# Performance work log

Measured on AMD Instinct MI355X. Metric: run time of the kernel, lower is better.

## Reference

```python
import jax, jax.numpy as jnp
import numpy as np

NUM_HEADS = 12
D_MODEL = 768
D_HEAD = D_MODEL // NUM_HEADS


def setup_inputs() -> dict:
    key = jax.random.key(0)
    k_x, k_wqkv, k_bqkv, k_wo, k_bo = jax.random.split(key, 5)
    B, S = 1, 4096
    x = jax.random.normal(k_x, (B, S, D_MODEL), dtype=jnp.float32)
    # flax Dense default init: lecun_normal for kernel, zeros for bias
    w_qkv = jax.random.normal(k_wqkv, (D_MODEL, 3 * D_MODEL), dtype=jnp.float32) / np.sqrt(D_MODEL)
    b_qkv = jnp.zeros((3 * D_MODEL,), dtype=jnp.float32)
    w_o = jax.random.normal(k_wo, (D_MODEL, D_MODEL), dtype=jnp.float32) / np.sqrt(D_MODEL)
    b_o = jnp.zeros((D_MODEL,), dtype=jnp.float32)
    return {"x": x, "w_qkv": w_qkv, "b_qkv": b_qkv, "w_o": w_o, "b_o": b_o}


def reference(x, w_qkv, b_qkv, w_o, b_o):
    B, S, _ = x.shape
    H, Dh = NUM_HEADS, D_HEAD
    qkv = jnp.einsum('bsd,de->bse', x, w_qkv) + b_qkv  # [B,S,3*D]
    q, k, v = jnp.split(qkv, 3, axis=-1)
    # [B,S,D] -> [B,H,S,Dh]
    q = q.reshape(B, S, H, Dh).transpose(0, 2, 1, 3)
    k = k.reshape(B, S, H, Dh).transpose(0, 2, 1, 3)
    v = v.reshape(B, S, H, Dh).transpose(0, 2, 1, 3)
    logits = jnp.einsum('bhqd,bhkd->bhqk', q, k) / jnp.sqrt(jnp.float32(Dh))
    weights = jax.nn.softmax(logits, axis=-1)  # deterministic=True -> no dropout
    attn = jnp.einsum('bhqk,bhkd->bhqd', weights, v)
    attn = attn.transpose(0, 2, 1, 3).reshape(B, S, H * Dh)
    return jnp.einsum('bsd,de->bse', attn, w_o) + b_o
```

## Files before the change

kernel.cpp:

```cpp
#include <hip/hip_runtime.h>

typedef unsigned short u16;
typedef __attribute__((ext_vector_type(8))) short bf16x8;
typedef __attribute__((ext_vector_type(4))) float f32x4;

#define CST 0.18033688011112042f

__device__ inline u16 f2bf(float f) {
    unsigned u;
    __builtin_memcpy(&u, &f, 4);
    unsigned r = (u + 0x7FFF + ((u >> 16) & 1)) >> 16;
    return (u16)r;
}
__device__ inline unsigned pack2(float lo, float hi) {
    return (unsigned)f2bf(lo) | ((unsigned)f2bf(hi) << 16);
}
__device__ inline unsigned fbits(float f) {
    unsigned u;
    __builtin_memcpy(&u, &f, 4);
    return u;
}
__device__ inline f32x4 fzero() {
    f32x4 z = {0.f, 0.f, 0.f, 0.f};
    return z;
}
__device__ inline f32x4 mfma16(bf16x8 a, bf16x8 b, f32x4 c) {
    return __builtin_amdgcn_mfma_f32_16x16x32_bf16(a, b, c, 0, 0, 0);
}

__device__ inline void gld_lds16(const u16* g, u16* l) {
    __builtin_amdgcn_global_load_lds(
        reinterpret_cast<const __attribute__((address_space(1))) unsigned int*>(
            reinterpret_cast<uintptr_t>(g)),
        reinterpret_cast<__attribute__((address_space(3))) unsigned int*>(
            static_cast<unsigned int>(reinterpret_cast<uintptr_t>(l))),
        16, 0, 0);
}

#define NB_WQKV (72 * 24)
#define NB_WO   (24 * 24)
#define NB_CVT  (4096 * 768 / 2048)

__global__ __launch_bounds__(256) void prep(const float* __restrict__ x,
                                            const float* __restrict__ w_qkv,
                                            const float* __restrict__ w_o,
                                            u16* __restrict__ xb,
                                            u16* __restrict__ wqkvT,
                                            u16* __restrict__ woT) {
    __shared__ float tile[32][33];
    int bid = blockIdx.x;
    int t = threadIdx.x;
    if (bid < NB_WQKV + NB_WO) {
        const float* in;
        u16* out;
        int bx, by, R, C;
        if (bid < NB_WQKV) {
            in = w_qkv; out = wqkvT; R = 768; C = 2304;
            bx = bid % 72; by = bid / 72;
        } else {
            int b2 = bid - NB_WQKV;
            in = w_o; out = woT; R = 768; C = 768;
            bx = b2 % 24; by = b2 / 24;
        }
        int c0 = bx * 32, r0 = by * 32;
        int tx = t & 31, ty = t >> 5;
#pragma unroll
        for (int j = 0; j < 32; j += 8)
            tile[ty + j][tx] = in[(size_t)(r0 + ty + j) * C + c0 + tx];
        __syncthreads();
#pragma unroll
        for (int j = 0; j < 32; j += 8)
            out[(size_t)(c0 + ty + j) * R + r0 + tx] = f2bf(tile[tx][ty + j]);
    } else {
        int i = (bid - NB_WQKV - NB_WO) * 2048 + t * 8;
        float4 a = *(const float4*)(x + i);
        float4 b = *(const float4*)(x + i + 4);
        uint4 w;
        w.x = pack2(a.x, a.y);
        w.y = pack2(a.z, a.w);
        w.z = pack2(b.x, b.y);
        w.w = pack2(b.z, b.w);
        *(uint4*)(xb + i) = w;
    }
}

__global__ __launch_bounds__(256) void vtrans(const u16* __restrict__ qkv,
                                              u16* __restrict__ vt) {
    __shared__ u16 T[64 * 136];
    int t = threadIdx.x;
    int h = blockIdx.y, kv0 = blockIdx.x * 128;
    {
        int key = t >> 1, ch = (t & 1) * 32;
        const u16* vp = qkv + (size_t)(kv0 + key) * 2304 + 1536 + h * 64 + ch;
        u16 tmp[32];
        *(uint4*)&tmp[0]  = *(const uint4*)vp;
        *(uint4*)&tmp[8]  = *(const uint4*)(vp + 8);
        *(uint4*)&tmp[16] = *(const uint4*)(vp + 16);
        *(uint4*)&tmp[24] = *(const uint4*)(vp + 24);
        int k5 = key & 31, grp = key >> 5;
        int kp = (grp << 5) | (((k5 >> 2) & 3) << 3) | ((k5 >> 4) << 2) | (k5 & 3);
#pragma unroll
        for (int j = 0; j < 32; j++) T[(ch + j) * 136 + kp] = tmp[j];
    }
    __syncthreads();
    {
        int dh = t >> 2, kc = (t & 3) * 32;
        uint4 o0 = *(const uint4*)&T[dh * 136 + kc];
        uint4 o1 = *(const uint4*)&T[dh * 136 + kc + 8];
        uint4 o2 = *(const uint4*)&T[dh * 136 + kc + 16];
        uint4 o3 = *(const uint4*)&T[dh * 136 + kc + 24];
        u16* op = vt + ((size_t)(h * 64 + dh)) * 4096 + kv0 + kc;
        *(uint4*)op = o0;
        *(uint4*)(op + 8) = o1;
        *(uint4*)(op + 16) = o2;
        *(uint4*)(op + 24) = o3;
    }
}

template <int MT, bool OUT_F32, bool SCALE_Q>
__global__ __launch_bounds__(256) void gemm_bt(const u16* __restrict__ A,
                                               const u16* __restrict__ Bt,
                                               const float* __restrict__ bias,
                                               void* __restrict__ Cv,
                                               int M, int N, int K) {
    constexpr int MI = MT / 32;
    constexpr int NA = MT / 64;
    constexpr int AH = MT * 32;
    constexpr int BH = 128 * 32;
    __shared__ u16 As[2 * AH];
    __shared__ u16 Bs[2 * BH];

    int t = threadIdx.x;
    int wave = t >> 6, lane = t & 63, quad = lane >> 4, l16 = lane & 15;
    int mbase = blockIdx.y * MT, nbase = blockIdx.x * 128;
    int mw = (wave & 1) * (MT / 2), nw = (wave >> 1) * 64;

    f32x4 acc[MI][4];
#pragma unroll
    for (int i = 0; i < MI; i++)
#pragma unroll
        for (int j = 0; j < 4; j++) acc[i][j] = fzero();

    int xqs = (lane & 3) ^ ((lane >> 3) & 3);
    const u16* AgL[NA];
    u16* AsL[NA];
#pragma unroll
    for (int j = 0; j < NA; j++) {
        int rl = wave * (MT / 4) + j * 16 + (lane >> 2);
        AgL[j] = A + (size_t)(mbase + rl) * K + xqs * 8;
        AsL[j] = As + wave * (MT / 4) * 32 + j * 512;
    }
    const u16* BgL[2];
    u16* BsL[2];
#pragma unroll
    for (int j = 0; j < 2; j++) {
        int rl = wave * 32 + j * 16 + (lane >> 2);
        BgL[j] = Bt + (size_t)(nbase + rl) * K + xqs * 8;
        BsL[j] = Bs + wave * 1024 + j * 512;
    }

    auto STAGE = [&](int buf, int kt) {
#pragma unroll
        for (int j = 0; j < NA; j++) gld_lds16(AgL[j] + kt, AsL[j] + buf * AH);
#pragma unroll
        for (int j = 0; j < 2; j++) gld_lds16(BgL[j] + kt, BsL[j] + buf * BH);
    };

    int xq = quad ^ ((l16 >> 1) & 3);
    int afo[MI], bfo[4];
#pragma unroll
    for (int i = 0; i < MI; i++) afo[i] = (mw + i * 16 + l16) * 32 + xq * 8;
#pragma unroll
    for (int i = 0; i < 4; i++) bfo[i] = (nw + i * 16 + l16) * 32 + xq * 8;

    STAGE(0, 0);
    __syncthreads();

    int cur = 0;
    for (int kt = 0; kt < K; kt += 32) {
        if (kt + 32 < K) STAGE(cur ^ 1, kt + 32);

        const u16* AsB = As + cur * AH;
        const u16* BsB = Bs + cur * BH;
        bf16x8 af[MI], bfr[4];
#pragma unroll
        for (int i = 0; i < MI; i++) af[i] = *(const bf16x8*)&AsB[afo[i]];
#pragma unroll
        for (int i = 0; i < 4; i++) bfr[i] = *(const bf16x8*)&BsB[bfo[i]];
#pragma unroll
        for (int mi = 0; mi < MI; mi++)
#pragma unroll
            for (int ni = 0; ni < 4; ni++)
                acc[mi][ni] = mfma16(af[mi], bfr[ni], acc[mi][ni]);

        __syncthreads();
        cur ^= 1;
    }

#pragma unroll
    for (int ni = 0; ni < 4; ni++) {
        int col = nbase + nw + ni * 16 + l16;
        float bv = bias[col];
        float scale = (SCALE_Q && col < 768) ? CST : 1.0f;
#pragma unroll
        for (int mi = 0; mi < MI; mi++) {
#pragma unroll
            for (int r = 0; r < 4; r++) {
                int row = mbase + mw + mi * 16 + quad * 4 + r;
                float v = (acc[mi][ni][r] + bv) * scale;
                if (OUT_F32)
                    ((float*)Cv)[(size_t)row * N + col] = v;
                else
                    ((u16*)Cv)[(size_t)row * N + col] = f2bf(v);
            }
        }
    }
}

#define SEQ 4096
#define QKV_LD 2304

__global__ __launch_bounds__(256, 4) void attn_flash(const u16* __restrict__ qkv,
                                                     const u16* __restrict__ vt,
                                                     u16* __restrict__ attn) {
    __shared__ __align__(16) char smem[32768];

    int t = threadIdx.x;
    int wave = t >> 6, lane = t & 63, quad = lane >> 4, l16 = lane & 15;
    int kw = wave & 1, qw = wave >> 1;
    int h = blockIdx.y;
    int q0 = blockIdx.x * 64;
    const int QOFF = h * 64, KOFF = 768 + h * 64;

    bf16x8 qf[2][2];
#pragma unroll
    for (int qs = 0; qs < 2; qs++) {
        const u16* qp = qkv + (size_t)(q0 + qw * 32 + qs * 16 + l16) * QKV_LD + QOFF + quad * 8;
        qf[qs][0] = *(const bf16x8*)(qp);
        qf[qs][1] = *(const bf16x8*)(qp + 32);
    }

    f32x4 o[2][4];
    float l4[2];
#pragma unroll
    for (int qs = 0; qs < 2; qs++) {
        l4[qs] = 0.f;
#pragma unroll
        for (int j = 0; j < 4; j++) o[qs][j] = fzero();
    }

    const u16* kgl[2];
    int kofs[2];
#pragma unroll
    for (int j = 0; j < 2; j++) {
        int r = wave * 16 + j * 8 + (lane >> 3);
        kgl[j] = qkv + (size_t)r * QKV_LD + KOFF +
                 (((lane & 7) ^ ((lane >> 3) & 7)) * 8);
        kofs[j] = (wave * 16 + j * 8) * 64;
    }
    const u16* vgl[2];
    int vofs[2];
#pragma unroll
    for (int j = 0; j < 2; j++) {
        int r = wave * 16 + j * 8 + (lane >> 3);
        vgl[j] = vt + (size_t)(h * 64 + r) * SEQ +
                 (((lane & 7) ^ ((lane >> 3) & 7)) * 8);
        vofs[j] = (wave * 16 + j * 8) * 64;
    }

    auto STAGE = [&](int buf, int kv) {
        u16* kb = (u16*)(smem + buf * 8192);
        u16* vb = (u16*)(smem + 16384 + buf * 8192);
#pragma unroll
        for (int j = 0; j < 2; j++) gld_lds16(kgl[j] + (size_t)kv * QKV_LD, kb + kofs[j]);
#pragma unroll
        for (int j = 0; j < 2; j++) gld_lds16(vgl[j] + kv, vb + vofs[j]);
    };

    STAGE(0, 0);
    __syncthreads();

    int cur = 0;
    int x7 = l16 & 7;
    for (int kv0 = 0; kv0 < SEQ; kv0 += 64) {
        if (kv0 + 64 < SEQ) STAGE(cur ^ 1, kv0 + 64);

        const u16* KsB = (const u16*)(smem + cur * 8192);
        const u16* VsB = (const u16*)(smem + 16384 + cur * 8192);

        bf16x8 kf[2][2];
#pragma unroll
        for (int st = 0; st < 2; st++) {
            int r = kw * 32 + st * 16 + l16;
            kf[st][0] = *(const bf16x8*)&KsB[r * 64 + (quad ^ x7) * 8];
            kf[st][1] = *(const bf16x8*)&KsB[r * 64 + ((quad + 4) ^ x7) * 8];
        }
        bf16x8 vf[4];
#pragma unroll
        for (int nt = 0; nt < 4; nt++) {
            int r = nt * 16 + l16;
            vf[nt] = *(const bf16x8*)&VsB[r * 64 + ((kw * 4 + quad) ^ x7) * 8];
        }

        __builtin_amdgcn_s_setprio(1);
#pragma unroll
        for (int qs = 0; qs < 2; qs++) {
            f32x4 s0 = mfma16(kf[0][0], qf[qs][0], fzero());
            s0 = mfma16(kf[0][1], qf[qs][1], s0);
            f32x4 s1 = mfma16(kf[1][0], qf[qs][0], fzero());
            s1 = mfma16(kf[1][1], qf[qs][1], s1);
            float p00 = exp2f(s0[0]), p01 = exp2f(s0[1]);
            float p02 = exp2f(s0[2]), p03 = exp2f(s0[3]);
            float p10 = exp2f(s1[0]), p11 = exp2f(s1[1]);
            float p12 = exp2f(s1[2]), p13 = exp2f(s1[3]);
            l4[qs] += ((p00 + p01) + (p02 + p03)) + ((p10 + p11) + (p12 + p13));
            uint4 pk;
            pk.x = __builtin_amdgcn_perm(fbits(p01), fbits(p00), 0x07060302u);
            pk.y = __builtin_amdgcn_perm(fbits(p03), fbits(p02), 0x07060302u);
            pk.z = __builtin_amdgcn_perm(fbits(p11), fbits(p10), 0x07060302u);
            pk.w = __builtin_amdgcn_perm(fbits(p13), fbits(p12), 0x07060302u);
            bf16x8 pf;
            __builtin_memcpy(&pf, &pk, 16);
#pragma unroll
            for (int nt = 0; nt < 4; nt++)
                o[qs][nt] = mfma16(pf, vf[nt], o[qs][nt]);
        }
        __builtin_amdgcn_s_setprio(0);

        __syncthreads();
        cur ^= 1;
    }

#pragma unroll
    for (int qs = 0; qs < 2; qs++) {
        l4[qs] += __shfl_xor(l4[qs], 16);
        l4[qs] += __shfl_xor(l4[qs], 32);
    }
    float* M0 = (float*)smem;
    float* Lm = (float*)(smem + 17408);
    if (lane < 16) {
        Lm[kw * 64 + qw * 32 + l16] = l4[0];
        Lm[kw * 64 + qw * 32 + 16 + l16] = l4[1];
    }
    if (kw == 1) {
#pragma unroll
        for (int nt = 0; nt < 4; nt++)
#pragma unroll
            for (int r = 0; r < 4; r++)
                M0[(qw * 32 + quad * 4 + r) * 68 + nt * 16 + l16] = o[0][nt][r];
    } else {
#pragma unroll
        for (int nt = 0; nt < 4; nt++)
#pragma unroll
            for (int r = 0; r < 4; r++)
                M0[(qw * 32 + 16 + quad * 4 + r) * 68 + nt * 16 + l16] = o[1][nt][r];
    }
    __syncthreads();
    if (kw == 0) {
#pragma unroll
        for (int r = 0; r < 4; r++) {
            int rw = qw * 32 + quad * 4 + r;
            float l = Lm[rw] + Lm[64 + rw];
            float inv = 1.0f / l;
            u16* op = attn + (size_t)(q0 + rw) * 768 + h * 64;
#pragma unroll
            for (int nt = 0; nt < 4; nt++) {
                float v = o[0][nt][r] + M0[rw * 68 + nt * 16 + l16];
                op[nt * 16 + l16] = f2bf(v * inv);
            }
        }
    } else {
#pragma unroll
        for (int r = 0; r < 4; r++) {
            int rw = qw * 32 + 16 + quad * 4 + r;
            float l = Lm[rw] + Lm[64 + rw];
            float inv = 1.0f / l;
            u16* op = attn + (size_t)(q0 + rw) * 768 + h * 64;
#pragma unroll
            for (int nt = 0; nt < 4; nt++) {
                float v = o[1][nt][r] + M0[rw * 68 + nt * 16 + l16];
                op[nt * 16 + l16] = f2bf(v * inv);
            }
        }
    }
}

extern "C" void kernel_launch(void* const* d_in, const int* in_sizes, int n_in,
                              void* d_out, int out_size, void* d_ws, size_t ws_size,
                              hipStream_t stream) {
    const float* x      = (const float*)d_in[0];
    const float* w_qkv  = (const float*)d_in[1];
    const float* b_qkv  = (const float*)d_in[2];
    const float* w_o    = (const float*)d_in[3];
    const float* b_o    = (const float*)d_in[4];
    float* out = (float*)d_out;

    u16* wqkvT = (u16*)d_ws;
    u16* woT   = wqkvT + (size_t)2304 * 768;
    u16* qkv   = woT + (size_t)768 * 768;
    u16* attnb = qkv + (size_t)4096 * 2304;
    u16* Vt    = attnb + (size_t)4096 * 768;
    u16* xb    = attnb;

    prep<<<dim3(NB_WQKV + NB_WO + NB_CVT), 256, 0, stream>>>(
        x, w_qkv, w_o, xb, wqkvT, woT);

    gemm_bt<128, false, true><<<dim3(2304 / 128, 4096 / 128), 256, 0, stream>>>(
        xb, wqkvT, b_qkv, qkv, 4096, 2304, 768);

    vtrans<<<dim3(SEQ / 128, 12), 256, 0, stream>>>(qkv, Vt);

    attn_flash<<<dim3(SEQ / 64, 12), 256, 0, stream>>>(qkv, Vt, attnb);

    gemm_bt<64, true, false><<<dim3(768 / 128, 4096 / 64), 256, 0, stream>>>(
        attnb, woT, b_o, out, 4096, 768, 768);
}
```

Baseline: 198.9 us.

## Compute softmax row sums via MFMA, use native exp2, swizzle block order

The attention kernel now accumulates softmax denominators with an extra MFMA against a vector of bf16 ones, instead of scalar adds plus cross-lane shuffles. It calls the raw hardware exp2 builtin to skip the libm wrapper. Both the GEMM and attention kernels remap block indices with an XCD-style swizzle so neighbouring tiles share L2. Row sums are now taken from bf16-rounded probabilities, matching the numerator, but one extra MFMA per tile adds matrix-core work. The GEMM swizzle assumes the grid size is divisible by 8.

After: 177.7 us. 1.12x faster.

```diff
diff --git a/kernel.cpp b/kernel.cpp
--- a/kernel.cpp
+++ b/kernel.cpp
@@ -5,6 +5,12 @@
 typedef __attribute__((ext_vector_type(4))) float f32x4;
 
 #define CST 0.18033688011112042f
+
+#if __has_builtin(__builtin_amdgcn_exp2f)
+#define EXP2(x) __builtin_amdgcn_exp2f(x)
+#else
+#define EXP2(x) exp2f(x)
+#endif
 
 __device__ inline u16 f2bf(float f) {
     unsigned u;
@@ -132,7 +138,14 @@
 
     int t = threadIdx.x;
     int wave = t >> 6, lane = t & 63, quad = lane >> 4, l16 = lane & 15;
-    int mbase = blockIdx.y * MT, nbase = blockIdx.x * 128;
+
+    int gx = gridDim.x;
+    int flat = blockIdx.y * gx + blockIdx.x;
+    int cpx = (gx * gridDim.y) >> 3;
+    int swz = (flat & 7) * cpx + (flat >> 3);
+    int bx = swz % gx, by = swz / gx;
+
+    int mbase = by * MT, nbase = bx * 128;
     int mw = (wave & 1) * (MT / 2), nw = (wave >> 1) * 64;
 
     f32x4 acc[MI][4];
@@ -228,8 +241,11 @@
     int t = threadIdx.x;
     int wave = t >> 6, lane = t & 63, quad = lane >> 4, l16 = lane & 15;
     int kw = wave & 1, qw = wave >> 1;
-    int h = blockIdx.y;
-    int q0 = blockIdx.x * 64;
+
+    int flat = blockIdx.y * 64 + blockIdx.x;
+    int swz = (flat & 7) * 96 + (flat >> 3);
+    int h = swz >> 6;
+    int q0 = (swz & 63) * 64;
     const int QOFF = h * 64, KOFF = 768 + h * 64;
 
     bf16x8 qf[2][2];
@@ -241,40 +257,36 @@
     }
 
     f32x4 o[2][4];
-    float l4[2];
+    f32x4 lacc[2];
 #pragma unroll
     for (int qs = 0; qs < 2; qs++) {
-        l4[qs] = 0.f;
+        lacc[qs] = fzero();
 #pragma unroll
         for (int j = 0; j < 4; j++) o[qs][j] = fzero();
     }
+    bf16x8 vones;
+#pragma unroll
+    for (int j = 0; j < 8; j++) vones[j] = (short)0x3F80;
 
     const u16* kgl[2];
-    int kofs[2];
+    const u16* vgl[2];
+    int sofs[2];
 #pragma unroll
     for (int j = 0; j < 2; j++) {
         int r = wave * 16 + j * 8 + (lane >> 3);
-        kgl[j] = qkv + (size_t)r * QKV_LD + KOFF +
-                 (((lane & 7) ^ ((lane >> 3) & 7)) * 8);
-        kofs[j] = (wave * 16 + j * 8) * 64;
-    }
-    const u16* vgl[2];
-    int vofs[2];
-#pragma unroll
-    for (int j = 0; j < 2; j++) {
-        int r = wave * 16 + j * 8 + (lane >> 3);
-        vgl[j] = vt + (size_t)(h * 64 + r) * SEQ +
-                 (((lane & 7) ^ ((lane >> 3) & 7)) * 8);
-        vofs[j] = (wave * 16 + j * 8) * 64;
+        int cd = (lane & 7) ^ ((lane >> 3) & 7);
+        kgl[j] = qkv + (size_t)r * QKV_LD + KOFF + cd * 8;
+        vgl[j] = vt + (size_t)(h * 64 + r) * SEQ + cd * 8;
+        sofs[j] = (wave * 16 + j * 8) * 64;
     }
 
     auto STAGE = [&](int buf, int kv) {
         u16* kb = (u16*)(smem + buf * 8192);
         u16* vb = (u16*)(smem + 16384 + buf * 8192);
 #pragma unroll
-        for (int j = 0; j < 2; j++) gld_lds16(kgl[j] + (size_t)kv * QKV_LD, kb + kofs[j]);
-#pragma unroll
-        for (int j = 0; j < 2; j++) gld_lds16(vgl[j] + kv, vb + vofs[j]);
+        for (int j = 0; j < 2; j++) gld_lds16(kgl[j] + (size_t)kv * QKV_LD, kb + sofs[j]);
+#pragma unroll
+        for (int j = 0; j < 2; j++) gld_lds16(vgl[j] + kv, vb + sofs[j]);
     };
 
     STAGE(0, 0);
@@ -309,11 +321,10 @@
             s0 = mfma16(kf[0][1], qf[qs][1], s0);
             f32x4 s1 = mfma16(kf[1][0], qf[qs][0], fzero());
             s1 = mfma16(kf[1][1], qf[qs][1], s1);
-            float p00 = exp2f(s0[0]), p01 = exp2f(s0[1]);
-            float p02 = exp2f(s0[2]), p03 = exp2f(s0[3]);
-            float p10 = exp2f(s1[0]), p11 = exp2f(s1[1]);
-            float p12 = exp2f(s1[2]), p13 = exp2f(s1[3]);
-            l4[qs] += ((p00 + p01) + (p02 + p03)) + ((p10 + p11) + (p12 + p13));
+            float p00 = EXP2(s0[0]), p01 = EXP2(s0[1]);
+            float p02 = EXP2(s0[2]), p03 = EXP2(s0[3]);
+            float p10 = EXP2(s1[0]), p11 = EXP2(s1[1]);
+            float p12 = EXP2(s1[2]), p13 = EXP2(s1[3]);
             uint4 pk;
             pk.x = __builtin_amdgcn_perm(fbits(p01), fbits(p00), 0x07060302u);
             pk.y = __builtin_amdgcn_perm(fbits(p03), fbits(p02), 0x07060302u);
@@ -321,6 +332,7 @@
             pk.w = __builtin_amdgcn_perm(fbits(p13), fbits(p12), 0x07060302u);
             bf16x8 pf;
             __builtin_memcpy(&pf, &pk, 16);
+            lacc[qs] = mfma16(pf, vones, lacc[qs]);
 #pragma unroll
             for (int nt = 0; nt < 4; nt++)
                 o[qs][nt] = mfma16(pf, vf[nt], o[qs][nt]);
@@ -331,16 +343,14 @@
         cur ^= 1;
     }
 
-#pragma unroll
-    for (int qs = 0; qs < 2; qs++) {
-        l4[qs] += __shfl_xor(l4[qs], 16);
-        l4[qs] += __shfl_xor(l4[qs], 32);
-    }
     float* M0 = (float*)smem;
     float* Lm = (float*)(smem + 17408);
-    if (lane < 16) {
-        Lm[kw * 64 + qw * 32 + l16] = l4[0];
-        Lm[kw * 64 + qw * 32 + 16 + l16] = l4[1];
+    if (l16 == 0) {
+#pragma unroll
+        for (int qs = 0; qs < 2; qs++)
+#pragma unroll
+            for (int r = 0; r < 4; r++)
+                Lm[kw * 64 + qw * 32 + qs * 16 + quad * 4 + r] = lacc[qs][r];
     }
     if (kw == 1) {
 #pragma unroll
@@ -360,8 +370,8 @@
 #pragma unroll
         for (int r = 0; r < 4; r++) {
             int rw = qw * 32 + quad * 4 + r;
-            float l = Lm[rw] + Lm[64 + rw];
-            float inv = 1.0f / l;
+            float ltot = Lm[rw] + Lm[64 + rw];
+            float inv = 1.0f / ltot;
             u16* op = attn + (size_t)(q0 + rw) * 768 + h * 64;
 #pragma unroll
             for (int nt = 0; nt < 4; nt++) {
@@ -373,8 +383,8 @@
 #pragma unroll
         for (int r = 0; r < 4; r++) {
             int rw = qw * 32 + 16 + quad * 4 + r;
-            float l = Lm[rw] + Lm[64 + rw];
-            float inv = 1.0f / l;
+            float ltot = Lm[rw] + Lm[64 + rw];
+            float inv = 1.0f / ltot;
             u16* op = attn + (size_t)(q0 + rw) * 768 + h * 64;
 #pragma unroll
             for (int nt = 0; nt < 4; nt++) {
```
